# Kernel tuning notes

Measured on AMD Instinct MI355X. Metric: run time of the kernel, lower is better.

The kernel has to match this reference:

```python
import jax, jax.numpy as jnp
import numpy as np
from jax.lax import associative_scan

D_H = 512

def _binary_operator(e_i, e_j):
    a_i, kv_i = e_i
    a_j, kv_j = e_j
    return (a_j * a_i, a_j * kv_i + kv_j)

def setup_inputs() -> dict:
    key = jax.random.key(0)
    x = jax.random.normal(key, (4, 8192, 3 * D_H), dtype=jnp.float32)
    return {"x": x}

def reference(x):
    d_h = x.shape[-1] // 3
    inp = jnp.tanh(x[:, :, :d_h])
    gates = jax.nn.sigmoid(x[:, :, d_h:])
    input_gate, output_gate = jnp.split(gates, 2, axis=-1)
    forget_gate = 1.0 - input_gate
    # diagonal linear recurrence h_t = f_t * h_{t-1} + i_t * x_t via associative scan
    _, hidden_state = associative_scan(_binary_operator, (forget_gate, inp * input_gate), axis=1)
    return jnp.tanh(hidden_state) * output_gate
```

## Files before the change

kernel.cpp:

```cpp
#include <hip/hip_runtime.h>


#define B_  4
#define T_  8192
#define DH_ 512
#define ROW_ 1536

typedef float f32x4 __attribute__((ext_vector_type(4)));

__device__ __forceinline__ float rcp_f(float x) {
    return __builtin_amdgcn_rcpf(x);
}
__device__ __forceinline__ float sigmoid_f(float x) {
    return rcp_f(1.0f + __expf(-x));
}
__device__ __forceinline__ float tanh_f(float x) {
    return 1.0f - 2.0f * rcp_f(__expf(2.0f * x) + 1.0f);
}

__global__ void k_partials(const float* __restrict__ x,
                           float* __restrict__ agg_a,
                           float* __restrict__ agg_kv,
                           int C, int Tc) {
    const int c = blockIdx.x;
    const int b = blockIdx.y;
    const int d = threadIdx.x << 2;
    const float* xb = x + ((size_t)b * T_ + (size_t)c * Tc) * ROW_;

    float A[4]  = {1.f, 1.f, 1.f, 1.f};
    float KV[4] = {0.f, 0.f, 0.f, 0.f};
#pragma unroll 8
    for (int i = 0; i < Tc; ++i) {
        const float* r = xb + (size_t)i * ROW_;
        const f32x4 xi = *(const f32x4*)(r + d);
        const f32x4 gi = *(const f32x4*)(r + DH_ + d);
#pragma unroll
        for (int j = 0; j < 4; ++j) {
            const float s  = sigmoid_f(gi[j]);
            const float f  = 1.0f - s;
            const float iv = tanh_f(xi[j]) * s;
            A[j]  = f * A[j];
            KV[j] = fmaf(f, KV[j], iv);
        }
    }
    const size_t idx = ((size_t)b * C + c) * DH_ + d;
    f32x4 Av  = {A[0],  A[1],  A[2],  A[3]};
    f32x4 KVv = {KV[0], KV[1], KV[2], KV[3]};
    *(f32x4*)(agg_a + idx)  = Av;
    *(f32x4*)(agg_kv + idx) = KVv;
}

__global__ void k_scan(const float* __restrict__ agg_a,
                       const float* __restrict__ agg_kv,
                       float* __restrict__ h0,
                       int C) {
    const int b = blockIdx.x;
    const int d = threadIdx.x << 2;
    float h[4] = {0.f, 0.f, 0.f, 0.f};
#pragma unroll 8
    for (int c = 0; c < C; ++c) {
        const size_t idx = ((size_t)b * C + c) * DH_ + d;
        f32x4 hv = {h[0], h[1], h[2], h[3]};
        *(f32x4*)(h0 + idx) = hv;
        const f32x4 a  = *(const f32x4*)(agg_a + idx);
        const f32x4 kv = *(const f32x4*)(agg_kv + idx);
#pragma unroll
        for (int j = 0; j < 4; ++j) h[j] = fmaf(a[j], h[j], kv[j]);
    }
}

__global__ void k_apply(const float* __restrict__ x,
                        const float* __restrict__ h0buf,
                        float* __restrict__ out,
                        int C, int Tc) {
    const int c = blockIdx.x;
    const int b = blockIdx.y;
    const int d = threadIdx.x << 2;

    float h[4] = {0.f, 0.f, 0.f, 0.f};
    if (h0buf) {
        const f32x4 hv = *(const f32x4*)(h0buf + ((size_t)b * C + c) * DH_ + d);
#pragma unroll
        for (int j = 0; j < 4; ++j) h[j] = hv[j];
    }

    const float* xb = x + ((size_t)b * T_ + (size_t)c * Tc) * ROW_;
    float* ob = out + ((size_t)b * T_ + (size_t)c * Tc) * DH_;

#pragma unroll 4
    for (int i = 0; i < Tc; ++i) {
        const float* r = xb + (size_t)i * ROW_;
        const f32x4 xi = *(const f32x4*)(r + d);
        const f32x4 gi = *(const f32x4*)(r + DH_ + d);
        const f32x4 go = *(const f32x4*)(r + 2 * DH_ + d);
        f32x4 o;
#pragma unroll
        for (int j = 0; j < 4; ++j) {
            const float s  = sigmoid_f(gi[j]);
            const float f  = 1.0f - s;
            const float iv = tanh_f(xi[j]) * s;
            h[j] = fmaf(f, h[j], iv);
            o[j] = tanh_f(h[j]) * sigmoid_f(go[j]);
        }
        __builtin_nontemporal_store(o, (f32x4*)(ob + (size_t)i * DH_ + d));
    }
}

extern "C" void kernel_launch(void* const* d_in, const int* in_sizes, int n_in,
                              void* d_out, int out_size, void* d_ws, size_t ws_size,
                              hipStream_t stream) {
    const float* x = (const float*)d_in[0];
    float* out = (float*)d_out;

    const dim3 blk(DH_ / 4);

    int C = 256;
    while (C > 1 && (size_t)B_ * C * DH_ * 3 * sizeof(float) > ws_size) C >>= 1;

    if (C == 1) {
        hipLaunchKernelGGL(k_apply, dim3(1, B_), blk, 0, stream,
                           x, (const float*)nullptr, out, 1, T_);
        return;
    }

    const int Tc = T_ / C;
    float* agg_a  = (float*)d_ws;
    float* agg_kv = agg_a  + (size_t)B_ * C * DH_;
    float* h0     = agg_kv + (size_t)B_ * C * DH_;

    const dim3 grid(C, B_);
    hipLaunchKernelGGL(k_partials, grid, blk, 0, stream, x, agg_a, agg_kv, C, Tc);
    hipLaunchKernelGGL(k_scan, dim3(B_), blk, 0, stream, agg_a, agg_kv, h0, C);
    hipLaunchKernelGGL(k_apply, grid, blk, 0, stream, x, h0, out, C, Tc);
}
```

Baseline: 328.6 us.

## Software-pipeline row loads, widen scan threads, and double chunk count

Adds explicit two-deep register prefetching of input rows in the partials and apply kernels so global loads for step i+2 are issued before step i is computed. The scan kernel now uses one thread per channel (512 threads) with a one-step prefetch of the aggregates, replacing the four-wide vector path. The chunk count grows from 256 to 512, giving more blocks and shorter per-chunk serial loops at the cost of a longer sequential scan and more workspace. The prefetching raises register pressure and may duplicate loads at the tail.

```diff
diff --git a/kernel.cpp b/kernel.cpp
--- a/kernel.cpp
+++ b/kernel.cpp
@@ -29,19 +29,29 @@
 
     float A[4]  = {1.f, 1.f, 1.f, 1.f};
     float KV[4] = {0.f, 0.f, 0.f, 0.f};
-#pragma unroll 8
+
+    f32x4 x0 = *(const f32x4*)(xb + d);
+    f32x4 g0 = *(const f32x4*)(xb + DH_ + d);
+    const float* r1 = xb + ROW_;
+    f32x4 x1 = *(const f32x4*)(r1 + d);
+    f32x4 g1 = *(const f32x4*)(r1 + DH_ + d);
+
+#pragma unroll 4
     for (int i = 0; i < Tc; ++i) {
-        const float* r = xb + (size_t)i * ROW_;
-        const f32x4 xi = *(const f32x4*)(r + d);
-        const f32x4 gi = *(const f32x4*)(r + DH_ + d);
+        const int ip = (i + 2 < Tc) ? (i + 2) : (Tc - 1);
+        const float* rp = xb + (size_t)ip * ROW_;
+        const f32x4 xn = *(const f32x4*)(rp + d);
+        const f32x4 gn = *(const f32x4*)(rp + DH_ + d);
 #pragma unroll
         for (int j = 0; j < 4; ++j) {
-            const float s  = sigmoid_f(gi[j]);
+            const float s  = sigmoid_f(g0[j]);
             const float f  = 1.0f - s;
-            const float iv = tanh_f(xi[j]) * s;
+            const float iv = tanh_f(x0[j]) * s;
             A[j]  = f * A[j];
             KV[j] = fmaf(f, KV[j], iv);
         }
+        x0 = x1; g0 = g1;
+        x1 = xn; g1 = gn;
     }
     const size_t idx = ((size_t)b * C + c) * DH_ + d;
     f32x4 Av  = {A[0],  A[1],  A[2],  A[3]};
@@ -55,17 +65,20 @@
                        float* __restrict__ h0,
                        int C) {
     const int b = blockIdx.x;
-    const int d = threadIdx.x << 2;
-    float h[4] = {0.f, 0.f, 0.f, 0.f};
-#pragma unroll 8
+    const int d = threadIdx.x;
+    const size_t base = (size_t)b * C * DH_ + d;
+
+    float h  = 0.f;
+    float ac = agg_a[base];
+    float kc = agg_kv[base];
+#pragma unroll 4
     for (int c = 0; c < C; ++c) {
-        const size_t idx = ((size_t)b * C + c) * DH_ + d;
-        f32x4 hv = {h[0], h[1], h[2], h[3]};
-        *(f32x4*)(h0 + idx) = hv;
-        const f32x4 a  = *(const f32x4*)(agg_a + idx);
-        const f32x4 kv = *(const f32x4*)(agg_kv + idx);
-#pragma unroll
-        for (int j = 0; j < 4; ++j) h[j] = fmaf(a[j], h[j], kv[j]);
+        const int cp = (c + 1 < C) ? (c + 1) : c;
+        const float an = agg_a[base + (size_t)cp * DH_];
+        const float kn = agg_kv[base + (size_t)cp * DH_];
+        h0[base + (size_t)c * DH_] = h;
+        h = fmaf(ac, h, kc);
+        ac = an; kc = kn;
     }
 }
 
@@ -87,22 +100,35 @@
     const float* xb = x + ((size_t)b * T_ + (size_t)c * Tc) * ROW_;
     float* ob = out + ((size_t)b * T_ + (size_t)c * Tc) * DH_;
 
+    f32x4 x0 = *(const f32x4*)(xb + d);
+    f32x4 g0 = *(const f32x4*)(xb + DH_ + d);
+    f32x4 o0 = *(const f32x4*)(xb + 2 * DH_ + d);
+    const float* r1 = xb + ROW_;
+    f32x4 x1 = *(const f32x4*)(r1 + d);
+    f32x4 g1 = *(const f32x4*)(r1 + DH_ + d);
+    f32x4 o1 = *(const f32x4*)(r1 + 2 * DH_ + d);
+
 #pragma unroll 4
     for (int i = 0; i < Tc; ++i) {
-        const float* r = xb + (size_t)i * ROW_;
-        const f32x4 xi = *(const f32x4*)(r + d);
-        const f32x4 gi = *(const f32x4*)(r + DH_ + d);
-        const f32x4 go = *(const f32x4*)(r + 2 * DH_ + d);
+        const int ip = (i + 2 < Tc) ? (i + 2) : (Tc - 1);
+        const float* rp = xb + (size_t)ip * ROW_;
+        const f32x4 xn = *(const f32x4*)(rp + d);
+        const f32x4 gn = *(const f32x4*)(rp + DH_ + d);
+        const f32x4 on = *(const f32x4*)(rp + 2 * DH_ + d);
+
         f32x4 o;
 #pragma unroll
         for (int j = 0; j < 4; ++j) {
-            const float s  = sigmoid_f(gi[j]);
+            const float s  = sigmoid_f(g0[j]);
             const float f  = 1.0f - s;
-            const float iv = tanh_f(xi[j]) * s;
+            const float iv = tanh_f(x0[j]) * s;
             h[j] = fmaf(f, h[j], iv);
-            o[j] = tanh_f(h[j]) * sigmoid_f(go[j]);
+            o[j] = tanh_f(h[j]) * sigmoid_f(o0[j]);
         }
         __builtin_nontemporal_store(o, (f32x4*)(ob + (size_t)i * DH_ + d));
+
+        x0 = x1; g0 = g1; o0 = o1;
+        x1 = xn; g1 = gn; o1 = on;
     }
 }
 
@@ -112,10 +138,10 @@
     const float* x = (const float*)d_in[0];
     float* out = (float*)d_out;
 
+    int C = 512;
+    while (C > 1 && (size_t)B_ * C * DH_ * 3 * sizeof(float) > ws_size) C >>= 1;
+
     const dim3 blk(DH_ / 4);
-
-    int C = 256;
-    while (C > 1 && (size_t)B_ * C * DH_ * 3 * sizeof(float) > ws_size) C >>= 1;
 
     if (C == 1) {
         hipLaunchKernelGGL(k_apply, dim3(1, B_), blk, 0, stream,
@@ -130,6 +156,6 @@
 
     const dim3 grid(C, B_);
     hipLaunchKernelGGL(k_partials, grid, blk, 0, stream, x, agg_a, agg_kv, C, Tc);
-    hipLaunchKernelGGL(k_scan, dim3(B_), blk, 0, stream, agg_a, agg_kv, h0, C);
+    hipLaunchKernelGGL(k_scan, dim3(B_), dim3(DH_), 0, stream, agg_a, agg_kv, h0, C);
     hipLaunchKernelGGL(k_apply, grid, blk, 0, stream, x, h0, out, C, Tc);
 }
```

New measurement: 369.4 us. +12.4%, slower.

## Parallelize chunk-carry scan with Hillis-Steele scan in shared memory

Applied to the files above, without the earlier changes.

Replaces the serial per-batch loop over 256 chunk aggregates, which ran on only 4 blocks, with a block-parallel Hillis-Steele scan. It now launches one block per (channel, batch) and one thread per chunk, combining affine pairs in shared memory. This targets the latency of the small serial middle stage. In exchange it does more total work (log C steps with two barriers each), and its global accesses are strided by DH_ and therefore uncoalesced.

```diff
diff --git a/kernel.cpp b/kernel.cpp
--- a/kernel.cpp
+++ b/kernel.cpp
@@ -54,19 +54,32 @@
                        const float* __restrict__ agg_kv,
                        float* __restrict__ h0,
                        int C) {
-    const int b = blockIdx.x;
-    const int d = threadIdx.x << 2;
-    float h[4] = {0.f, 0.f, 0.f, 0.f};
-#pragma unroll 8
-    for (int c = 0; c < C; ++c) {
-        const size_t idx = ((size_t)b * C + c) * DH_ + d;
-        f32x4 hv = {h[0], h[1], h[2], h[3]};
-        *(f32x4*)(h0 + idx) = hv;
-        const f32x4 a  = *(const f32x4*)(agg_a + idx);
-        const f32x4 kv = *(const f32x4*)(agg_kv + idx);
-#pragma unroll
-        for (int j = 0; j < 4; ++j) h[j] = fmaf(a[j], h[j], kv[j]);
+    __shared__ float sa[1024];
+    __shared__ float sk[1024];
+    const int d = blockIdx.x;
+    const int b = blockIdx.y;
+    const int c = threadIdx.x;
+
+    const size_t idx = ((size_t)b * C + c) * DH_ + d;
+    float am = agg_a[idx];
+    float km = agg_kv[idx];
+    sa[c] = am;
+    sk[c] = km;
+    __syncthreads();
+
+    for (int o = 1; o < C; o <<= 1) {
+        float ap = 1.f, kp = 0.f;
+        if (c >= o) { ap = sa[c - o]; kp = sk[c - o]; }
+        __syncthreads();
+        km = fmaf(am, kp, km);
+        am = am * ap;
+        sa[c] = am;
+        sk[c] = km;
+        __syncthreads();
     }
+
+    const float h = (c == 0) ? 0.f : sk[c - 1];
+    h0[idx] = h;
 }
 
 __global__ void k_apply(const float* __restrict__ x,
@@ -130,6 +143,7 @@
 
     const dim3 grid(C, B_);
     hipLaunchKernelGGL(k_partials, grid, blk, 0, stream, x, agg_a, agg_kv, C, Tc);
-    hipLaunchKernelGGL(k_scan, dim3(B_), blk, 0, stream, agg_a, agg_kv, h0, C);
+    hipLaunchKernelGGL(k_scan, dim3(DH_, B_), dim3(C), 0, stream,
+                       agg_a, agg_kv, h0, C);
     hipLaunchKernelGGL(k_apply, grid, blk, 0, stream, x, h0, out, C, Tc);
 }
```

Measured after the change: 316.2 us. -3.8%, faster.

## Fuse three-pass chunked scan into one cooperative kernel with parallel carry scan

Applied to the files above, without the earlier changes.

Replaces the partials, serial carry scan and apply kernels with one cooperative kernel that uses grid-wide syncs between phases. The carry scan across the 256 chunks becomes a shared-memory Hillis-Steele scan, with each block handling two channels, instead of a 4-block serial loop over chunks. This removes two launch boundaries and the long serial scan. In exchange it needs all 1024 blocks co-resident, adds two grid barriers, and the partials and apply phases can no longer overlap.

```diff
diff --git a/kernel.cpp b/kernel.cpp
--- a/kernel.cpp
+++ b/kernel.cpp
@@ -1,10 +1,15 @@
 #include <hip/hip_runtime.h>
+#include <hip/hip_cooperative_groups.h>
+
+namespace cg = cooperative_groups;
 
 
-#define B_  4
-#define T_  8192
-#define DH_ 512
+#define B_   4
+#define T_   8192
+#define DH_  512
 #define ROW_ 1536
+#define C_   256
+#define TC_  32
 
 typedef float f32x4 __attribute__((ext_vector_type(4)));
 
@@ -18,81 +23,113 @@
     return 1.0f - 2.0f * rcp_f(__expf(2.0f * x) + 1.0f);
 }
 
-__global__ void k_partials(const float* __restrict__ x,
-                           float* __restrict__ agg_a,
-                           float* __restrict__ agg_kv,
-                           int C, int Tc) {
-    const int c = blockIdx.x;
-    const int b = blockIdx.y;
-    const int d = threadIdx.x << 2;
-    const float* xb = x + ((size_t)b * T_ + (size_t)c * Tc) * ROW_;
+__global__ __launch_bounds__(128, 2)
+void k_fused(const float* __restrict__ x,
+             float* __restrict__ out,
+             float* __restrict__ agg_a,
+             float* __restrict__ agg_kv,
+             float* __restrict__ h0) {
+    const int c  = blockIdx.x;
+    const int b  = blockIdx.y;
+    const int d4 = threadIdx.x << 2;
+    const int t  = threadIdx.x;
 
-    float A[4]  = {1.f, 1.f, 1.f, 1.f};
-    float KV[4] = {0.f, 0.f, 0.f, 0.f};
+    __shared__ float sa[128];
+    __shared__ float sk[128];
+
+    const float* xb = x + ((size_t)b * T_ + (size_t)c * TC_) * ROW_;
+
+    {
+        float A[4] = {1.f, 1.f, 1.f, 1.f};
+        float K[4] = {0.f, 0.f, 0.f, 0.f};
 #pragma unroll 8
-    for (int i = 0; i < Tc; ++i) {
-        const float* r = xb + (size_t)i * ROW_;
-        const f32x4 xi = *(const f32x4*)(r + d);
-        const f32x4 gi = *(const f32x4*)(r + DH_ + d);
+        for (int i = 0; i < TC_; ++i) {
+            const float* r = xb + (size_t)i * ROW_;
+            const f32x4 xi = *(const f32x4*)(r + d4);
+            const f32x4 gi = *(const f32x4*)(r + DH_ + d4);
 #pragma unroll
-        for (int j = 0; j < 4; ++j) {
-            const float s  = sigmoid_f(gi[j]);
-            const float f  = 1.0f - s;
-            const float iv = tanh_f(xi[j]) * s;
-            A[j]  = f * A[j];
-            KV[j] = fmaf(f, KV[j], iv);
+            for (int j = 0; j < 4; ++j) {
+                const float s  = sigmoid_f(gi[j]);
+                const float f  = 1.0f - s;
+                const float iv = tanh_f(xi[j]) * s;
+                A[j] = f * A[j];
+                K[j] = fmaf(f, K[j], iv);
+            }
         }
+        const size_t idx = ((size_t)b * C_ + c) * DH_ + d4;
+        f32x4 Av = {A[0], A[1], A[2], A[3]};
+        f32x4 Kv = {K[0], K[1], K[2], K[3]};
+        *(f32x4*)(agg_a + idx)  = Av;
+        *(f32x4*)(agg_kv + idx) = Kv;
     }
-    const size_t idx = ((size_t)b * C + c) * DH_ + d;
-    f32x4 Av  = {A[0],  A[1],  A[2],  A[3]};
-    f32x4 KVv = {KV[0], KV[1], KV[2], KV[3]};
-    *(f32x4*)(agg_a + idx)  = Av;
-    *(f32x4*)(agg_kv + idx) = KVv;
-}
 
-__global__ void k_scan(const float* __restrict__ agg_a,
-                       const float* __restrict__ agg_kv,
-                       float* __restrict__ h0,
-                       int C) {
-    const int b = blockIdx.x;
-    const int d = threadIdx.x << 2;
-    float h[4] = {0.f, 0.f, 0.f, 0.f};
-#pragma unroll 8
-    for (int c = 0; c < C; ++c) {
-        const size_t idx = ((size_t)b * C + c) * DH_ + d;
-        f32x4 hv = {h[0], h[1], h[2], h[3]};
-        *(f32x4*)(h0 + idx) = hv;
-        const f32x4 a  = *(const f32x4*)(agg_a + idx);
-        const f32x4 kv = *(const f32x4*)(agg_kv + idx);
+    cg::this_grid().sync();
+
+    for (int half = 0; half < 2; ++half) {
+        const int d = (c << 1) | half;
+        const size_t i0 = ((size_t)b * C_ + 2 * t)     * DH_ + d;
+        const size_t i1 = ((size_t)b * C_ + 2 * t + 1) * DH_ + d;
+        const float a0 = agg_a[i0], k0 = agg_kv[i0];
+        const float a1 = agg_a[i1], k1 = agg_kv[i1];
+        float am = a1 * a0;
+        float km = fmaf(a1, k0, k1);
+        __syncthreads();
+        sa[t] = am; sk[t] = km;
+        __syncthreads();
+        for (int o = 1; o < 128; o <<= 1) {
+            float ap = 1.f, kp = 0.f;
+            if (t >= o) { ap = sa[t - o]; kp = sk[t - o]; }
+            __syncthreads();
+            km = fmaf(am, kp, km);
+            am = am * ap;
+            sa[t] = am; sk[t] = km;
+            __syncthreads();
+        }
+        const float ke = (t > 0) ? sk[t - 1] : 0.f;
+        h0[i0] = ke;
+        h0[i1] = fmaf(a0, ke, k0);
+    }
+
+    cg::this_grid().sync();
+
+    {
+        float h[4];
+        const f32x4 hv = *(const f32x4*)(h0 + ((size_t)b * C_ + c) * DH_ + d4);
 #pragma unroll
-        for (int j = 0; j < 4; ++j) h[j] = fmaf(a[j], h[j], kv[j]);
+        for (int j = 0; j < 4; ++j) h[j] = hv[j];
+
+        float* ob = out + ((size_t)b * T_ + (size_t)c * TC_) * DH_;
+#pragma unroll 4
+        for (int i = 0; i < TC_; ++i) {
+            const float* r = xb + (size_t)i * ROW_;
+            const f32x4 xi = *(const f32x4*)(r + d4);
+            const f32x4 gi = *(const f32x4*)(r + DH_ + d4);
+            const f32x4 go = *(const f32x4*)(r + 2 * DH_ + d4);
+            f32x4 o;
+#pragma unroll
+            for (int j = 0; j < 4; ++j) {
+                const float s  = sigmoid_f(gi[j]);
+                const float f  = 1.0f - s;
+                const float iv = tanh_f(xi[j]) * s;
+                h[j] = fmaf(f, h[j], iv);
+                o[j] = tanh_f(h[j]) * sigmoid_f(go[j]);
+            }
+            __builtin_nontemporal_store(o, (f32x4*)(ob + (size_t)i * DH_ + d4));
+        }
     }
 }
 
-__global__ void k_apply(const float* __restrict__ x,
-                        const float* __restrict__ h0buf,
-                        float* __restrict__ out,
-                        int C, int Tc) {
-    const int c = blockIdx.x;
-    const int b = blockIdx.y;
-    const int d = threadIdx.x << 2;
-
+__global__ void k_seq(const float* __restrict__ x, float* __restrict__ out) {
+    const int b = blockIdx.x;
+    const int d4 = threadIdx.x << 2;
+    const float* xb = x + (size_t)b * T_ * ROW_;
+    float* ob = out + (size_t)b * T_ * DH_;
     float h[4] = {0.f, 0.f, 0.f, 0.f};
-    if (h0buf) {
-        const f32x4 hv = *(const f32x4*)(h0buf + ((size_t)b * C + c) * DH_ + d);
-#pragma unroll
-        for (int j = 0; j < 4; ++j) h[j] = hv[j];
-    }
-
-    const float* xb = x + ((size_t)b * T_ + (size_t)c * Tc) * ROW_;
-    float* ob = out + ((size_t)b * T_ + (size_t)c * Tc) * DH_;
-
-#pragma unroll 4
-    for (int i = 0; i < Tc; ++i) {
+    for (int i = 0; i < T_; ++i) {
         const float* r = xb + (size_t)i * ROW_;
-        const f32x4 xi = *(const f32x4*)(r + d);
-        const f32x4 gi = *(const f32x4*)(r + DH_ + d);
-        const f32x4 go = *(const f32x4*)(r + 2 * DH_ + d);
+        const f32x4 xi = *(const f32x4*)(r + d4);
+        const f32x4 gi = *(const f32x4*)(r + DH_ + d4);
+        const f32x4 go = *(const f32x4*)(r + 2 * DH_ + d4);
         f32x4 o;
 #pragma unroll
         for (int j = 0; j < 4; ++j) {
@@ -102,7 +139,7 @@
             h[j] = fmaf(f, h[j], iv);
             o[j] = tanh_f(h[j]) * sigmoid_f(go[j]);
         }
-        __builtin_nontemporal_store(o, (f32x4*)(ob + (size_t)i * DH_ + d));
+        *(f32x4*)(ob + (size_t)i * DH_ + d4) = o;
     }
 }
 
@@ -112,24 +149,18 @@
     const float* x = (const float*)d_in[0];
     float* out = (float*)d_out;
 
-    const dim3 blk(DH_ / 4);
-
-    int C = 256;
-    while (C > 1 && (size_t)B_ * C * DH_ * 3 * sizeof(float) > ws_size) C >>= 1;
-
-    if (C == 1) {
-        hipLaunchKernelGGL(k_apply, dim3(1, B_), blk, 0, stream,
-                           x, (const float*)nullptr, out, 1, T_);
+    const size_t n_agg = (size_t)B_ * C_ * DH_;
+    if (ws_size < 3 * n_agg * sizeof(float)) {
+        hipLaunchKernelGGL(k_seq, dim3(B_), dim3(DH_ / 4), 0, stream, x, out);
         return;
     }
 
-    const int Tc = T_ / C;
     float* agg_a  = (float*)d_ws;
-    float* agg_kv = agg_a  + (size_t)B_ * C * DH_;
-    float* h0     = agg_kv + (size_t)B_ * C * DH_;
+    float* agg_kv = agg_a  + n_agg;
+    float* h0     = agg_kv + n_agg;
 
-    const dim3 grid(C, B_);
-    hipLaunchKernelGGL(k_partials, grid, blk, 0, stream, x, agg_a, agg_kv, C, Tc);
-    hipLaunchKernelGGL(k_scan, dim3(B_), blk, 0, stream, agg_a, agg_kv, h0, C);
-    hipLaunchKernelGGL(k_apply, grid, blk, 0, stream, x, h0, out, C, Tc);
+    void* kargs[] = {(void*)&x, (void*)&out, (void*)&agg_a,
+                     (void*)&agg_kv, (void*)&h0};
+    hipLaunchCooperativeKernel((const void*)k_fused, dim3(C_, B_), dim3(128),
+                               kargs, 0, stream);
 }
```

New measurement: 551.4 us. 67.8% more time.
